# Kernel optimization log

Measured on AMD Instinct MI355X. Metric: run time of the kernel, lower is better.

Reference implementation:

```python
import jax, jax.numpy as jnp
import numpy as np

TEMPERATURE = 0.8
TOP_P = 0.4
TOP_K = 50

BATCH = 256
VOCAB = 128000


def setup_inputs() -> dict:
    key = jax.random.key(0)
    logits = jax.random.normal(key, (BATCH, VOCAB), dtype=jnp.float32) * 3.0
    return {"logits": logits}


def _apply_top_p_top_k(logits, top_p, top_k):
    # sort descending; keep permutation so we can scatter the mask back
    sort_idx = jnp.argsort(-logits, axis=-1)                       # [B, V]
    logits_sort = jnp.take_along_axis(logits, sort_idx, axis=-1)   # [B, V]
    # top-p: mask tokens whose cumulative prob (excluding self) exceeds p
    probs_sort = jax.nn.softmax(logits_sort, axis=-1)
    probs_sum = jnp.cumsum(probs_sort, axis=-1)
    top_p_mask = (probs_sum - probs_sort) > top_p                  # [B, V]
    # top-k: mask everything past rank k in the sorted order
    top_k_mask = jnp.arange(logits.shape[-1]) >= top_k             # [V]
    masked = jnp.where(top_p_mask | top_k_mask, -jnp.inf, logits_sort)
    # invert the sort permutation and restore original token order
    inv_idx = jnp.argsort(sort_idx, axis=-1)
    return jnp.take_along_axis(masked, inv_idx, axis=-1)


def reference(logits) -> jnp.ndarray:
    # temperature scaling (original does in-place div when T != 1.0)
    logits = logits / jnp.asarray(TEMPERATURE, dtype=logits.dtype)
    logits = _apply_top_p_top_k(logits, TOP_P, TOP_K)
    probs = jax.nn.softmax(logits.astype(jnp.float32), axis=-1)
    logprobs = jax.nn.log_softmax(logits.astype(jnp.float32), axis=-1)  # computed as in original (unused in return)
    pred_token_idx = jnp.argmax(probs, axis=-1)[:, None]           # [B, 1]
    return pred_token_idx
```

## Files before the change

kernel.cpp:

```cpp
#include <hip/hip_runtime.h>


#define VOCAB 128000
#define NT4   (VOCAB / 4)
#define BLK   1024
#define NFULL (NT4 / (BLK * 4))

#define NEG_INF (-3.402823466e+38f)

__device__ __forceinline__ void upd(float v, int idx, float& b, int& bi) {
    if (v > b) { b = v; bi = idx; }
}

__device__ __forceinline__ void upd4(const float4& v, int base, float& b, int& bi) {
    upd(v.x, base + 0, b, bi);
    upd(v.y, base + 1, b, bi);
    upd(v.z, base + 2, b, bi);
    upd(v.w, base + 3, b, bi);
}

__global__ __launch_bounds__(BLK, 1) void argmax_rows(
    const float* __restrict__ logits, int* __restrict__ out) {
    const int row = blockIdx.x;
    const int tid = threadIdx.x;
    const float4* __restrict__ rowp =
        reinterpret_cast<const float4*>(logits + (size_t)row * VOCAB);

    float b0 = NEG_INF, b1 = NEG_INF, b2 = NEG_INF, b3 = NEG_INF;
    int   i0 = 0x7fffffff, i1 = 0x7fffffff, i2 = 0x7fffffff, i3 = 0x7fffffff;

    int i = tid;
    #pragma unroll 1
    for (int it = 0; it < NFULL; ++it, i += 4 * BLK) {
        float4 v0 = rowp[i];
        float4 v1 = rowp[i + BLK];
        float4 v2 = rowp[i + 2 * BLK];
        float4 v3 = rowp[i + 3 * BLK];
        upd4(v0, (i) << 2,            b0, i0);
        upd4(v1, (i + BLK) << 2,      b1, i1);
        upd4(v2, (i + 2 * BLK) << 2,  b2, i2);
        upd4(v3, (i + 3 * BLK) << 2,  b3, i3);
    }
    for (; i < NT4; i += BLK) {
        float4 v = rowp[i];
        upd4(v, i << 2, b0, i0);
    }

    float best = b0; int bestIdx = i0;
    if (b1 > best || (b1 == best && i1 < bestIdx)) { best = b1; bestIdx = i1; }
    if (b2 > best || (b2 == best && i2 < bestIdx)) { best = b2; bestIdx = i2; }
    if (b3 > best || (b3 == best && i3 < bestIdx)) { best = b3; bestIdx = i3; }

    #pragma unroll
    for (int off = 32; off > 0; off >>= 1) {
        float ov = __shfl_down(best, off, 64);
        int   oi = __shfl_down(bestIdx, off, 64);
        if (ov > best || (ov == best && oi < bestIdx)) { best = ov; bestIdx = oi; }
    }

    __shared__ float s_val[16];
    __shared__ int   s_idx[16];
    const int lane = tid & 63;
    const int wave = tid >> 6;
    if (lane == 0) { s_val[wave] = best; s_idx[wave] = bestIdx; }
    __syncthreads();

    if (wave == 0) {
        float v  = (lane < 16) ? s_val[lane] : NEG_INF;
        int   ix = (lane < 16) ? s_idx[lane] : 0x7fffffff;
        #pragma unroll
        for (int off = 8; off > 0; off >>= 1) {
            float ov = __shfl_down(v, off, 64);
            int   oi = __shfl_down(ix, off, 64);
            if (ov > v || (ov == v && oi < ix)) { v = ov; ix = oi; }
        }
        if (lane == 0) out[row] = ix;
    }
}

extern "C" void kernel_launch(void* const* d_in, const int* in_sizes, int n_in,
                              void* d_out, int out_size, void* d_ws, size_t ws_size,
                              hipStream_t stream) {
    const float* logits = (const float*)d_in[0];
    int* out = (int*)d_out;
    argmax_rows<<<out_size, BLK, 0, stream>>>(logits, out);
}
```

Measured before the change: 184.0 us.

## Split each row's argmax across eight blocks with a second reduction kernel

Replaces the one-1024-thread-block-per-row argmax with a two-stage reduction. The first kernel launches 2048 blocks of 256 threads, each reducing one eighth of a row into a (value, index) pair in the workspace. A small second kernel merges the eight partials per row, keeping lowest-index tie-breaking. The aim is more blocks in flight and higher occupancy so memory latency is better hidden, at the cost of an extra launch and a workspace round trip. The old single-kernel path remains as a fallback when the workspace is too small.

```diff
diff --git a/kernel.cpp b/kernel.cpp
--- a/kernel.cpp
+++ b/kernel.cpp
@@ -1,10 +1,13 @@
 #include <hip/hip_runtime.h>
 
 
-#define VOCAB 128000
-#define NT4   (VOCAB / 4)
-#define BLK   1024
-#define NFULL (NT4 / (BLK * 4))
+#define VOCAB  128000
+#define BATCH  256
+#define NSLICE 8
+#define SLICE_ELEMS (VOCAB / NSLICE)
+#define SLICE_F4    (SLICE_ELEMS / 4)
+#define BLK1   256
+#define NFULL1 (SLICE_F4 / (BLK1 * 4))
 
 #define NEG_INF (-3.402823466e+38f)
 
@@ -18,6 +21,90 @@
     upd(v.z, base + 2, b, bi);
     upd(v.w, base + 3, b, bi);
 }
+
+__global__ __launch_bounds__(BLK1, 8) void argmax_partial(
+    const float* __restrict__ logits, int2* __restrict__ part) {
+    const int row   = blockIdx.x >> 3;
+    const int slice = blockIdx.x & 7;
+    const float4* __restrict__ p = reinterpret_cast<const float4*>(
+        logits + (size_t)row * VOCAB + slice * SLICE_ELEMS);
+    const int cbase = slice * SLICE_ELEMS;
+
+    float b0 = NEG_INF, b1 = NEG_INF, b2 = NEG_INF, b3 = NEG_INF;
+    int   i0 = 0x7fffffff, i1 = 0x7fffffff, i2 = 0x7fffffff, i3 = 0x7fffffff;
+
+    int j = threadIdx.x;
+    #pragma unroll 1
+    for (int it = 0; it < NFULL1; ++it, j += 4 * BLK1) {
+        float4 v0 = p[j];
+        float4 v1 = p[j + BLK1];
+        float4 v2 = p[j + 2 * BLK1];
+        float4 v3 = p[j + 3 * BLK1];
+        upd4(v0, cbase + ((j) << 2),            b0, i0);
+        upd4(v1, cbase + ((j + BLK1) << 2),     b1, i1);
+        upd4(v2, cbase + ((j + 2 * BLK1) << 2), b2, i2);
+        upd4(v3, cbase + ((j + 3 * BLK1) << 2), b3, i3);
+    }
+    for (; j < SLICE_F4; j += BLK1) {
+        float4 v = p[j];
+        upd4(v, cbase + (j << 2), b0, i0);
+    }
+
+    float best = b0; int bestIdx = i0;
+    if (b1 > best || (b1 == best && i1 < bestIdx)) { best = b1; bestIdx = i1; }
+    if (b2 > best || (b2 == best && i2 < bestIdx)) { best = b2; bestIdx = i2; }
+    if (b3 > best || (b3 == best && i3 < bestIdx)) { best = b3; bestIdx = i3; }
+
+    #pragma unroll
+    for (int off = 32; off > 0; off >>= 1) {
+        float ov = __shfl_down(best, off, 64);
+        int   oi = __shfl_down(bestIdx, off, 64);
+        if (ov > best || (ov == best && oi < bestIdx)) { best = ov; bestIdx = oi; }
+    }
+
+    __shared__ float s_val[4];
+    __shared__ int   s_idx[4];
+    const int lane = threadIdx.x & 63;
+    const int wave = threadIdx.x >> 6;
+    if (lane == 0) { s_val[wave] = best; s_idx[wave] = bestIdx; }
+    __syncthreads();
+
+    if (wave == 0) {
+        float v  = (lane < 4) ? s_val[lane] : NEG_INF;
+        int   ix = (lane < 4) ? s_idx[lane] : 0x7fffffff;
+        #pragma unroll
+        for (int off = 2; off > 0; off >>= 1) {
+            float ov = __shfl_down(v, off, 64);
+            int   oi = __shfl_down(ix, off, 64);
+            if (ov > v || (ov == v && oi < ix)) { v = ov; ix = oi; }
+        }
+        if (lane == 0) part[blockIdx.x] = make_int2(__float_as_int(v), ix);
+    }
+}
+
+__global__ __launch_bounds__(64, 1) void argmax_final(
+    const int2* __restrict__ part, int* __restrict__ out) {
+    const int row  = blockIdx.x;
+    const int lane = threadIdx.x;
+    float v  = NEG_INF;
+    int   ix = 0x7fffffff;
+    if (lane < NSLICE) {
+        int2 e = part[row * NSLICE + lane];
+        v  = __int_as_float(e.x);
+        ix = e.y;
+    }
+    #pragma unroll
+    for (int off = 4; off > 0; off >>= 1) {
+        float ov = __shfl_down(v, off, 64);
+        int   oi = __shfl_down(ix, off, 64);
+        if (ov > v || (ov == v && oi < ix)) { v = ov; ix = oi; }
+    }
+    if (lane == 0) out[row] = ix;
+}
+
+#define BLK   1024
+#define NT4   (VOCAB / 4)
+#define NFULL (NT4 / (BLK * 4))
 
 __global__ __launch_bounds__(BLK, 1) void argmax_rows(
     const float* __restrict__ logits, int* __restrict__ out) {
@@ -83,5 +170,12 @@
                               hipStream_t stream) {
     const float* logits = (const float*)d_in[0];
     int* out = (int*)d_out;
-    argmax_rows<<<out_size, BLK, 0, stream>>>(logits, out);
+    const size_t need_ws = (size_t)BATCH * NSLICE * sizeof(int2);
+    if (ws_size >= need_ws && d_ws != nullptr) {
+        int2* part = (int2*)d_ws;
+        argmax_partial<<<BATCH * NSLICE, BLK1, 0, stream>>>(logits, part);
+        argmax_final<<<BATCH, 64, 0, stream>>>(part, out);
+    } else {
+        argmax_rows<<<BATCH, BLK, 0, stream>>>(logits, out);
+    }
 }
```

Result: slower. 188.7 us (+2.5%).
